# Optimization experiments

Hardware: AMD Instinct MI355X
Metric: run time of the kernel (lower is better)

The kernel has to match this reference:

```python
import jax, jax.numpy as jnp
import numpy as np

N_NODES = 100_000
N_EDGES = 1_000_000
LATENT = 64
HID_ATOM = 256
HID_BOND = 256
RBF_DIM = 32
RBF_DMAX = 10.0
N_ATOM_TYPES = 10
N_CHARGES = 6
N_BOND_ORDERS = 5


def setup_inputs() -> dict:
    key = jax.random.key(0)
    ks = jax.random.split(key, 12)
    positions = jax.random.normal(ks[0], (N_NODES, 3), dtype=jnp.float32) * 5.0
    quantized = jax.random.normal(ks[1], (N_NODES, LATENT), dtype=jnp.float32)
    pair_indices = jax.random.randint(ks[2], (N_EDGES, 2), 0, N_NODES, dtype=jnp.int64)
    s = 0.05
    return {
        "positions": positions,
        "quantized": quantized,
        "pair_indices": pair_indices,
        "aW1": jax.random.normal(ks[3], (LATENT, HID_ATOM), jnp.float32) * s,
        "ab1": jnp.zeros((HID_ATOM,), jnp.float32),
        "aW2": jax.random.normal(ks[4], (HID_ATOM, N_ATOM_TYPES + N_CHARGES), jnp.float32) * s,
        "ab2": jnp.zeros((N_ATOM_TYPES + N_CHARGES,), jnp.float32),
        "bW1": jax.random.normal(ks[5], (LATENT + RBF_DIM, HID_BOND), jnp.float32) * s,
        "bb1": jnp.zeros((HID_BOND,), jnp.float32),
        "bW2": jax.random.normal(ks[6], (HID_BOND, N_BOND_ORDERS), jnp.float32) * s,
        "bb2": jnp.zeros((N_BOND_ORDERS,), jnp.float32),
    }


def _norm_no_nan(x, eps=1e-8):
    # L2 norm over last axis, clamped to avoid NaN gradients at 0
    return jnp.sqrt(jnp.maximum(jnp.sum(x * x, axis=-1), eps))


def _rbf(D, D_min=0.0, D_max=RBF_DMAX, D_count=RBF_DIM):
    mu = jnp.linspace(D_min, D_max, D_count, dtype=D.dtype)  # [D_count]
    sigma = (D_max - D_min) / D_count
    z = (D[..., None] - mu) / sigma
    return jnp.exp(-z * z)  # [E, D_count]


def reference(positions, quantized, pair_indices, aW1, ab1, aW2, ab2, bW1, bb1, bW2, bb2):
    src = pair_indices[:, 0]
    dst = pair_indices[:, 1]
    # pairwise distances -> RBF expansion
    x_i = positions[src]            # [E, 3]
    x_j = positions[dst]
    dists = _rbf(_norm_no_nan(x_i - x_j))  # [E, rbf_dim]
    # atom decoder (per node)
    h = jax.nn.relu(quantized @ aW1 + ab1)
    scalar_logits = h @ aW2 + ab2
    atom_type_logits = scalar_logits[:, :N_ATOM_TYPES]
    atom_charge_logits = scalar_logits[:, N_ATOM_TYPES:]
    # bond decoder (per edge): gathered latent sum concat RBF
    pair_feats = quantized[src] + quantized[dst]           # [E, latent]
    combined = jnp.concatenate([pair_feats, dists], axis=1)  # [E, latent+rbf]
    hb = jax.nn.relu(combined @ bW1 + bb1)
    bond_order_logits = hb @ bW2 + bb2
    return (atom_type_logits, atom_charge_logits, bond_order_logits)
```

## Files before the change

### kernel.cpp

```cpp
#include <hip/hip_runtime.h>
#include <hip/hip_bf16.h>

typedef __bf16 bf16x8 __attribute__((ext_vector_type(8)));
typedef __bf16 bf16x4 __attribute__((ext_vector_type(4)));
typedef float  f32x4  __attribute__((ext_vector_type(4)));

#define N_NODES 100000
#define N_EDGES 1000000
#define LATENT  64
#define HID     256
#define RBF_DIM 32
#define NTYPES  10
#define NCHG    6
#define NBOND   5

#define ATOM_TILES (N_NODES / 32)
#define ANBLK 512

#define ETILE  64
#define ETILES (N_EDGES / ETILE)
#define ENBLK  512

__global__ __launch_bounds__(256) void prep_kernel(
    const float* __restrict__ q, __bf16* __restrict__ qb)
{
    const int i = blockIdx.x * 256 + threadIdx.x;
    const float4 a = *(const float4*)(q + (size_t)i * 8);
    const float4 b = *(const float4*)(q + (size_t)i * 8 + 4);
    bf16x8 v;
    v[0] = (__bf16)a.x; v[1] = (__bf16)a.y; v[2] = (__bf16)a.z; v[3] = (__bf16)a.w;
    v[4] = (__bf16)b.x; v[5] = (__bf16)b.y; v[6] = (__bf16)b.z; v[7] = (__bf16)b.w;
    *(bf16x8*)(qb + (size_t)i * 8) = v;
}

struct __align__(16) ASmem {
    __bf16 qs[32][72];
    __bf16 hsE[32][264];
    float  red[4][2][4][64];
};

__global__ __launch_bounds__(256, 2) void atom_kernel(
    const float* __restrict__ q,   const float* __restrict__ aW1,
    const float* __restrict__ ab1, const float* __restrict__ aW2,
    const float* __restrict__ ab2, float* __restrict__ outA,
    float* __restrict__ outB)
{
    __shared__ ASmem sm;
    const int t    = threadIdx.x;
    const int w    = t >> 6;
    const int lane = t & 63;
    const int l15  = lane & 15;
    const int hi   = lane >> 4;
    const int wcol = w * 64;

    bf16x8 aw1f[2][4];
    #pragma unroll
    for (int kb = 0; kb < 2; ++kb)
        #pragma unroll
        for (int nt = 0; nt < 4; ++nt) {
            const int nn = wcol + nt * 16 + l15;
            const int k0 = kb * 32 + hi * 8;
            bf16x8 v;
            #pragma unroll
            for (int j = 0; j < 8; ++j) v[j] = (__bf16)aW1[(k0 + j) * HID + nn];
            aw1f[kb][nt] = v;
        }
    bf16x8 aw2f[2];
    #pragma unroll
    for (int kk = 0; kk < 2; ++kk) {
        const int k0 = (w * 2 + kk) * 32 + hi * 8;
        bf16x8 v;
        #pragma unroll
        for (int j = 0; j < 8; ++j) v[j] = (__bf16)aW2[(k0 + j) * 16 + l15];
        aw2f[kk] = v;
    }
    float4 b1v[4];
    #pragma unroll
    for (int nt = 0; nt < 4; ++nt)
        b1v[nt] = *(const float4*)(&ab1[wcol + nt * 16 + hi * 4]);

    const int m_st = t >> 3;
    const int p_st = t & 7;

    for (int tile = blockIdx.x; tile < ATOM_TILES; tile += ANBLK) {
        const int node0 = tile * 32;
        {
            const float* qr = q + (size_t)(node0 + m_st) * 64 + p_st * 8;
            const float4 a0 = *(const float4*)(qr);
            const float4 a1 = *(const float4*)(qr + 4);
            bf16x8 v;
            v[0] = (__bf16)a0.x; v[1] = (__bf16)a0.y; v[2] = (__bf16)a0.z; v[3] = (__bf16)a0.w;
            v[4] = (__bf16)a1.x; v[5] = (__bf16)a1.y; v[6] = (__bf16)a1.z; v[7] = (__bf16)a1.w;
            *(bf16x8*)(&sm.qs[m_st][p_st * 8]) = v;
        }
        __syncthreads();

        f32x4 acc[2][4];
        #pragma unroll
        for (int mt = 0; mt < 2; ++mt)
            #pragma unroll
            for (int nt = 0; nt < 4; ++nt) {
                f32x4 z = {0.f, 0.f, 0.f, 0.f};
                acc[mt][nt] = z;
            }
        #pragma unroll
        for (int kb = 0; kb < 2; ++kb)
            #pragma unroll
            for (int mt = 0; mt < 2; ++mt) {
                const bf16x8 bq = *(const bf16x8*)((const char*)&sm.qs[0][0]
                                   + (mt * 16 + l15) * 144 + kb * 64 + hi * 16);
                #pragma unroll
                for (int nt = 0; nt < 4; ++nt)
                    acc[mt][nt] = __builtin_amdgcn_mfma_f32_16x16x32_bf16(
                        aw1f[kb][nt], bq, acc[mt][nt], 0, 0, 0);
            }
        #pragma unroll
        for (int mt = 0; mt < 2; ++mt)
            #pragma unroll
            for (int nt = 0; nt < 4; ++nt) {
                bf16x4 hv;
                #pragma unroll
                for (int r = 0; r < 4; ++r)
                    hv[r] = (__bf16)fmaxf(acc[mt][nt][r] + ((const float*)&b1v[nt])[r], 0.f);
                *(bf16x4*)(&sm.hsE[mt * 16 + l15][wcol + nt * 16 + hi * 4]) = hv;
            }
        __syncthreads();

        f32x4 acc2[2];
        {
            f32x4 z = {0.f, 0.f, 0.f, 0.f};
            acc2[0] = z; acc2[1] = z;
        }
        #pragma unroll
        for (int mt = 0; mt < 2; ++mt)
            #pragma unroll
            for (int kk = 0; kk < 2; ++kk) {
                const int kb = w * 2 + kk;
                const bf16x8 af = *(const bf16x8*)((const char*)&sm.hsE[0][0]
                                   + (mt * 16 + l15) * 528 + kb * 64 + hi * 16);
                acc2[mt] = __builtin_amdgcn_mfma_f32_16x16x32_bf16(
                    af, aw2f[kk], acc2[mt], 0, 0, 0);
            }
        #pragma unroll
        for (int mt = 0; mt < 2; ++mt)
            #pragma unroll
            for (int r = 0; r < 4; ++r)
                sm.red[w][mt][r][lane] = acc2[mt][r];
        __syncthreads();

        {
            const int o  = t & 15;
            const int m0 = t >> 4;
            #pragma unroll
            for (int half = 0; half < 2; ++half) {
                const int m  = m0 + half * 16;
                const int mt = m >> 4, rr = m & 15;
                const int hh = rr >> 2, r = rr & 3;
                float s = ab2[o];
                #pragma unroll
                for (int ww = 0; ww < 4; ++ww) s += sm.red[ww][mt][r][hh * 16 + o];
                const int node = node0 + m;
                if (o < NTYPES) outA[node * NTYPES + o] = s;
                else            outB[node * NCHG + (o - NTYPES)] = s;
            }
        }
        __syncthreads();
    }
}

struct __align__(16) ESmem {
    __bf16 comb[ETILE][104];
    __bf16 hsE[ETILE][264];
    __bf16 w2t[16][264];
};

template<bool USEBF>
__global__ __launch_bounds__(512, 4) void edge_kernel(
    const float* __restrict__ pos, const float* __restrict__ qf,
    const __bf16* __restrict__ qb, const int* __restrict__ pair,
    const float* __restrict__ bW1, const float* __restrict__ bb1,
    const float* __restrict__ bW2, const float* __restrict__ bb2,
    float* __restrict__ outC)
{
    __shared__ ESmem sm;
    const int t    = threadIdx.x;
    const int w    = t >> 6;
    const int lane = t & 63;
    const int l15  = lane & 15;
    const int hi   = lane >> 4;
    const int wcol = w * 32;

    {
        const int o  = t >> 5;
        const int k0 = (t & 31) * 8;
        bf16x8 v;
        #pragma unroll
        for (int j = 0; j < 8; ++j)
            v[j] = (o < NBOND) ? (__bf16)bW2[(k0 + j) * NBOND + o] : (__bf16)0.f;
        *(bf16x8*)(&sm.w2t[o][k0]) = v;
    }

    bf16x8 bw1f[3][2];
    #pragma unroll
    for (int kb = 0; kb < 3; ++kb)
        #pragma unroll
        for (int nt = 0; nt < 2; ++nt) {
            const int nn = wcol + nt * 16 + l15;
            const int k0 = kb * 32 + hi * 8;
            bf16x8 v;
            #pragma unroll
            for (int j = 0; j < 8; ++j) v[j] = (__bf16)bW1[(k0 + j) * HID + nn];
            bw1f[kb][nt] = v;
        }
    float4 b1v[2];
    b1v[0] = *(const float4*)(&bb1[wcol + hi * 4]);
    b1v[1] = *(const float4*)(&bb1[wcol + 16 + hi * 4]);
    const float bb2v = (l15 < NBOND) ? bb2[l15] : 0.f;

    const int e_loc = t >> 3;
    const int p     = t & 7;

    int tile = blockIdx.x;
    int2 pA = ((const int2*)pair)[(size_t)tile * ETILE + e_loc];
    bf16x8 gs, gd;
    float4 fs0, fs1, fd0, fd1;
    float  ps0, ps1, ps2, pd0, pd1, pd2;
    if constexpr (USEBF) {
        gs = *(const bf16x8*)(qb + (size_t)pA.x * 64 + p * 8);
        gd = *(const bf16x8*)(qb + (size_t)pA.y * 64 + p * 8);
    } else {
        fs0 = *(const float4*)(qf + (size_t)pA.x * 64 + p * 8);
        fs1 = *(const float4*)(qf + (size_t)pA.x * 64 + p * 8 + 4);
        fd0 = *(const float4*)(qf + (size_t)pA.y * 64 + p * 8);
        fd1 = *(const float4*)(qf + (size_t)pA.y * 64 + p * 8 + 4);
    }
    ps0 = pos[(size_t)pA.x * 3];  ps1 = pos[(size_t)pA.x * 3 + 1];  ps2 = pos[(size_t)pA.x * 3 + 2];
    pd0 = pos[(size_t)pA.y * 3];  pd1 = pos[(size_t)pA.y * 3 + 1];  pd2 = pos[(size_t)pA.y * 3 + 2];
    {
        const int tn = tile + ENBLK;
        pA = ((const int2*)pair)[(tn < ETILES ? (size_t)tn * ETILE : 0) + e_loc];
    }
    __syncthreads();

    for (; tile < ETILES; tile += ENBLK) {
        const int e0 = tile * ETILE;

        {
            bf16x8 cv;
            if constexpr (USEBF) {
                #pragma unroll
                for (int j = 0; j < 8; ++j)
                    cv[j] = (__bf16)((float)gs[j] + (float)gd[j]);
            } else {
                cv[0] = (__bf16)(fs0.x + fd0.x); cv[1] = (__bf16)(fs0.y + fd0.y);
                cv[2] = (__bf16)(fs0.z + fd0.z); cv[3] = (__bf16)(fs0.w + fd0.w);
                cv[4] = (__bf16)(fs1.x + fd1.x); cv[5] = (__bf16)(fs1.y + fd1.y);
                cv[6] = (__bf16)(fs1.z + fd1.z); cv[7] = (__bf16)(fs1.w + fd1.w);
            }
            *(bf16x8*)(&sm.comb[e_loc][p * 8]) = cv;

            const float dx = ps0 - pd0, dy = ps1 - pd1, dz = ps2 - pd2;
            const float D  = sqrtf(fmaxf(dx * dx + dy * dy + dz * dz, 1e-8f));
            bf16x4 rv;
            #pragma unroll
            for (int j = 0; j < 4; ++j) {
                const float mu = (float)(p * 4 + j) * (10.0f / 31.0f);
                const float z  = (D - mu) * 3.2f;
                rv[j] = (__bf16)__expf(-z * z);
            }
            *(bf16x4*)(&sm.comb[e_loc][64 + p * 4]) = rv;
        }
        __syncthreads();

        {
            const int2 pN = pA;
            if constexpr (USEBF) {
                gs = *(const bf16x8*)(qb + (size_t)pN.x * 64 + p * 8);
                gd = *(const bf16x8*)(qb + (size_t)pN.y * 64 + p * 8);
            } else {
                fs0 = *(const float4*)(qf + (size_t)pN.x * 64 + p * 8);
                fs1 = *(const float4*)(qf + (size_t)pN.x * 64 + p * 8 + 4);
                fd0 = *(const float4*)(qf + (size_t)pN.y * 64 + p * 8);
                fd1 = *(const float4*)(qf + (size_t)pN.y * 64 + p * 8 + 4);
            }
            ps0 = pos[(size_t)pN.x * 3];  ps1 = pos[(size_t)pN.x * 3 + 1];  ps2 = pos[(size_t)pN.x * 3 + 2];
            pd0 = pos[(size_t)pN.y * 3];  pd1 = pos[(size_t)pN.y * 3 + 1];  pd2 = pos[(size_t)pN.y * 3 + 2];
            const int tnn = tile + 2 * ENBLK;
            pA = ((const int2*)pair)[(tnn < ETILES ? (size_t)tnn * ETILE : 0) + e_loc];
        }

        f32x4 acc[4][2];
        #pragma unroll
        for (int mt = 0; mt < 4; ++mt)
            #pragma unroll
            for (int nt = 0; nt < 2; ++nt) {
                f32x4 z = {0.f, 0.f, 0.f, 0.f};
                acc[mt][nt] = z;
            }
        #pragma unroll
        for (int kb = 0; kb < 3; ++kb)
            #pragma unroll
            for (int mt = 0; mt < 4; ++mt) {
                const bf16x8 bf = *(const bf16x8*)((const char*)&sm.comb[0][0]
                                   + (mt * 16 + l15) * 208 + kb * 64 + hi * 16);
                acc[mt][0] = __builtin_amdgcn_mfma_f32_16x16x32_bf16(
                    bw1f[kb][0], bf, acc[mt][0], 0, 0, 0);
                acc[mt][1] = __builtin_amdgcn_mfma_f32_16x16x32_bf16(
                    bw1f[kb][1], bf, acc[mt][1], 0, 0, 0);
            }
        #pragma unroll
        for (int mt = 0; mt < 4; ++mt)
            #pragma unroll
            for (int nt = 0; nt < 2; ++nt) {
                bf16x4 hv;
                #pragma unroll
                for (int r = 0; r < 4; ++r)
                    hv[r] = (__bf16)fmaxf(acc[mt][nt][r] + ((const float*)&b1v[nt])[r], 0.f);
                *(bf16x4*)((char*)&sm.hsE[0][0]
                           + (mt * 16 + l15) * 528 + (wcol + nt * 16 + hi * 4) * 2) = hv;
            }
        __syncthreads();

        if (w < 4) {
            f32x4 a2a = {0.f, 0.f, 0.f, 0.f};
            f32x4 a2b = {0.f, 0.f, 0.f, 0.f};
            #pragma unroll
            for (int kk = 0; kk < 8; kk += 2) {
                const bf16x8 af0 = *(const bf16x8*)((const char*)&sm.hsE[0][0]
                                    + (w * 16 + l15) * 528 + kk * 64 + hi * 16);
                const bf16x8 bf0 = *(const bf16x8*)((const char*)&sm.w2t[0][0]
                                    + l15 * 528 + kk * 64 + hi * 16);
                a2a = __builtin_amdgcn_mfma_f32_16x16x32_bf16(af0, bf0, a2a, 0, 0, 0);
                const bf16x8 af1 = *(const bf16x8*)((const char*)&sm.hsE[0][0]
                                    + (w * 16 + l15) * 528 + (kk + 1) * 64 + hi * 16);
                const bf16x8 bf1 = *(const bf16x8*)((const char*)&sm.w2t[0][0]
                                    + l15 * 528 + (kk + 1) * 64 + hi * 16);
                a2b = __builtin_amdgcn_mfma_f32_16x16x32_bf16(af1, bf1, a2b, 0, 0, 0);
            }
            if (l15 < NBOND) {
                #pragma unroll
                for (int r = 0; r < 4; ++r)
                    outC[(size_t)(e0 + w * 16 + hi * 4 + r) * NBOND + l15]
                        = a2a[r] + a2b[r] + bb2v;
            }
        }
    }
}

extern "C" void kernel_launch(void* const* d_in, const int* in_sizes, int n_in,
                              void* d_out, int out_size, void* d_ws, size_t ws_size,
                              hipStream_t stream)
{
    const float* pos = (const float*)d_in[0];
    const float* q   = (const float*)d_in[1];
    const int*   pair= (const int*)  d_in[2];
    const float* aW1 = (const float*)d_in[3];
    const float* ab1 = (const float*)d_in[4];
    const float* aW2 = (const float*)d_in[5];
    const float* ab2 = (const float*)d_in[6];
    const float* bW1 = (const float*)d_in[7];
    const float* bb1 = (const float*)d_in[8];
    const float* bW2 = (const float*)d_in[9];
    const float* bb2 = (const float*)d_in[10];

    float* out  = (float*)d_out;
    float* outA = out;
    float* outB = out + (size_t)N_NODES * NTYPES;
    float* outC = out + (size_t)N_NODES * (NTYPES + NCHG);

    const size_t qb_bytes = (size_t)N_NODES * LATENT * sizeof(__bf16);
    const bool use_bf = (ws_size >= qb_bytes);
    __bf16* qb = (__bf16*)d_ws;

    if (use_bf)
        hipLaunchKernelGGL(prep_kernel, dim3(N_NODES * LATENT / (256 * 8)), dim3(256),
                           0, stream, q, qb);

    hipLaunchKernelGGL(atom_kernel, dim3(ANBLK), dim3(256), 0, stream,
                       q, aW1, ab1, aW2, ab2, outA, outB);

    if (use_bf)
        hipLaunchKernelGGL(edge_kernel<true>, dim3(ENBLK), dim3(512), 0, stream,
                           pos, q, qb, pair, bW1, bb1, bW2, bb2, outC);
    else
        hipLaunchKernelGGL(edge_kernel<false>, dim3(ENBLK), dim3(512), 0, stream,
                           pos, q, qb, pair, bW1, bb1, bW2, bb2, outC);
}
```

Baseline: 101.9 us.

## Swizzle edge-kernel LDS layouts, retile waves to 2x4, use lightweight barriers

Replaces the padded LDS rows in the edge kernel with unpadded power-of-two rows and XOR swizzling to avoid bank conflicts. It also changes the per-wave work split from 4 M-tiles by 2 N-tiles to 2 M-tiles by 4 N-tiles, so each comb fragment read from LDS feeds more MFMAs, at the cost of holding more weight fragments in registers. __syncthreads is replaced with an explicit lgkmcnt wait plus s_barrier, and the first barrier now sits after the next-tile gather loads are issued. The larger bw1f register array may pressure occupancy under the 512-thread, 4-block launch bounds.

```diff
diff --git a/kernel.cpp b/kernel.cpp
--- a/kernel.cpp
+++ b/kernel.cpp
@@ -169,10 +169,15 @@
 }
 
 struct __align__(16) ESmem {
-    __bf16 comb[ETILE][104];
-    __bf16 hsE[ETILE][264];
-    __bf16 w2t[16][264];
+    __bf16 comb[ETILE][128];
+    __bf16 hsE[ETILE][256];
+    __bf16 w2t[16][256];
 };
+
+__device__ __forceinline__ void bar_lgkm() {
+    asm volatile("s_waitcnt lgkmcnt(0)" ::: "memory");
+    __builtin_amdgcn_s_barrier();
+}
 
 template<bool USEBF>
 __global__ __launch_bounds__(512, 4) void edge_kernel(
@@ -188,37 +193,41 @@
     const int lane = t & 63;
     const int l15  = lane & 15;
     const int hi   = lane >> 4;
-    const int wcol = w * 32;
+    const int hid0 = (w & 3) * 64;
+    const int emg  = (w >> 2) * 32;
+    const int swz  = (l15 & 7) << 4;
 
     {
         const int o  = t >> 5;
-        const int k0 = (t & 31) * 8;
+        const int kq = t & 31;
         bf16x8 v;
         #pragma unroll
         for (int j = 0; j < 8; ++j)
-            v[j] = (o < NBOND) ? (__bf16)bW2[(k0 + j) * NBOND + o] : (__bf16)0.f;
-        *(bf16x8*)(&sm.w2t[o][k0]) = v;
-    }
-
-    bf16x8 bw1f[3][2];
+            v[j] = (o < NBOND) ? (__bf16)bW2[(kq * 8 + j) * NBOND + o] : (__bf16)0.f;
+        *(bf16x8*)((char*)&sm.w2t[0][0] + o * 512 + ((kq * 16) ^ ((o & 7) << 4))) = v;
+    }
+
+    bf16x8 bw1f[3][4];
     #pragma unroll
     for (int kb = 0; kb < 3; ++kb)
         #pragma unroll
-        for (int nt = 0; nt < 2; ++nt) {
-            const int nn = wcol + nt * 16 + l15;
+        for (int nt = 0; nt < 4; ++nt) {
+            const int nn = hid0 + nt * 16 + l15;
             const int k0 = kb * 32 + hi * 8;
             bf16x8 v;
             #pragma unroll
             for (int j = 0; j < 8; ++j) v[j] = (__bf16)bW1[(k0 + j) * HID + nn];
             bw1f[kb][nt] = v;
         }
-    float4 b1v[2];
-    b1v[0] = *(const float4*)(&bb1[wcol + hi * 4]);
-    b1v[1] = *(const float4*)(&bb1[wcol + 16 + hi * 4]);
+    float4 b1v[4];
+    #pragma unroll
+    for (int nt = 0; nt < 4; ++nt)
+        b1v[nt] = *(const float4*)(&bb1[hid0 + nt * 16 + hi * 4]);
     const float bb2v = (l15 < NBOND) ? bb2[l15] : 0.f;
 
     const int e_loc = t >> 3;
     const int p     = t & 7;
+    const int wswz  = (e_loc & 7) << 4;
 
     int tile = blockIdx.x;
     int2 pA = ((const int2*)pair)[(size_t)tile * ETILE + e_loc];
@@ -257,7 +266,7 @@
                 cv[4] = (__bf16)(fs1.x + fd1.x); cv[5] = (__bf16)(fs1.y + fd1.y);
                 cv[6] = (__bf16)(fs1.z + fd1.z); cv[7] = (__bf16)(fs1.w + fd1.w);
             }
-            *(bf16x8*)(&sm.comb[e_loc][p * 8]) = cv;
+            *(bf16x8*)((char*)&sm.comb[0][0] + e_loc * 256 + ((p * 16) ^ wswz)) = cv;
 
             const float dx = ps0 - pd0, dy = ps1 - pd1, dz = ps2 - pd2;
             const float D  = sqrtf(fmaxf(dx * dx + dy * dy + dz * dz, 1e-8f));
@@ -268,9 +277,8 @@
                 const float z  = (D - mu) * 3.2f;
                 rv[j] = (__bf16)__expf(-z * z);
             }
-            *(bf16x4*)(&sm.comb[e_loc][64 + p * 4]) = rv;
-        }
-        __syncthreads();
+            *(bf16x4*)((char*)&sm.comb[0][0] + e_loc * 256 + ((128 + p * 8) ^ wswz)) = rv;
+        }
 
         {
             const int2 pN = pA;
@@ -288,38 +296,41 @@
             const int tnn = tile + 2 * ENBLK;
             pA = ((const int2*)pair)[(tnn < ETILES ? (size_t)tnn * ETILE : 0) + e_loc];
         }
-
-        f32x4 acc[4][2];
-        #pragma unroll
-        for (int mt = 0; mt < 4; ++mt)
-            #pragma unroll
-            for (int nt = 0; nt < 2; ++nt) {
+        bar_lgkm();
+
+        f32x4 acc[2][4];
+        #pragma unroll
+        for (int mt = 0; mt < 2; ++mt)
+            #pragma unroll
+            for (int nt = 0; nt < 4; ++nt) {
                 f32x4 z = {0.f, 0.f, 0.f, 0.f};
                 acc[mt][nt] = z;
             }
         #pragma unroll
         for (int kb = 0; kb < 3; ++kb)
             #pragma unroll
-            for (int mt = 0; mt < 4; ++mt) {
+            for (int mt = 0; mt < 2; ++mt) {
                 const bf16x8 bf = *(const bf16x8*)((const char*)&sm.comb[0][0]
-                                   + (mt * 16 + l15) * 208 + kb * 64 + hi * 16);
-                acc[mt][0] = __builtin_amdgcn_mfma_f32_16x16x32_bf16(
-                    bw1f[kb][0], bf, acc[mt][0], 0, 0, 0);
-                acc[mt][1] = __builtin_amdgcn_mfma_f32_16x16x32_bf16(
-                    bw1f[kb][1], bf, acc[mt][1], 0, 0, 0);
-            }
-        #pragma unroll
-        for (int mt = 0; mt < 4; ++mt)
-            #pragma unroll
-            for (int nt = 0; nt < 2; ++nt) {
+                                   + (emg + mt * 16 + l15) * 256
+                                   + ((kb * 64 + hi * 16) ^ swz));
+                #pragma unroll
+                for (int nt = 0; nt < 4; ++nt)
+                    acc[mt][nt] = __builtin_amdgcn_mfma_f32_16x16x32_bf16(
+                        bw1f[kb][nt], bf, acc[mt][nt], 0, 0, 0);
+            }
+        #pragma unroll
+        for (int mt = 0; mt < 2; ++mt)
+            #pragma unroll
+            for (int nt = 0; nt < 4; ++nt) {
                 bf16x4 hv;
                 #pragma unroll
                 for (int r = 0; r < 4; ++r)
                     hv[r] = (__bf16)fmaxf(acc[mt][nt][r] + ((const float*)&b1v[nt])[r], 0.f);
                 *(bf16x4*)((char*)&sm.hsE[0][0]
-                           + (mt * 16 + l15) * 528 + (wcol + nt * 16 + hi * 4) * 2) = hv;
-            }
-        __syncthreads();
+                           + (emg + mt * 16 + l15) * 512
+                           + ((hid0 * 2 + nt * 32 + hi * 8) ^ swz)) = hv;
+            }
+        bar_lgkm();
 
         if (w < 4) {
             f32x4 a2a = {0.f, 0.f, 0.f, 0.f};
@@ -327,14 +338,14 @@
             #pragma unroll
             for (int kk = 0; kk < 8; kk += 2) {
                 const bf16x8 af0 = *(const bf16x8*)((const char*)&sm.hsE[0][0]
-                                    + (w * 16 + l15) * 528 + kk * 64 + hi * 16);
+                                    + (w * 16 + l15) * 512 + ((kk * 64 + hi * 16) ^ swz));
                 const bf16x8 bf0 = *(const bf16x8*)((const char*)&sm.w2t[0][0]
-                                    + l15 * 528 + kk * 64 + hi * 16);
+                                    + l15 * 512 + ((kk * 64 + hi * 16) ^ swz));
                 a2a = __builtin_amdgcn_mfma_f32_16x16x32_bf16(af0, bf0, a2a, 0, 0, 0);
                 const bf16x8 af1 = *(const bf16x8*)((const char*)&sm.hsE[0][0]
-                                    + (w * 16 + l15) * 528 + (kk + 1) * 64 + hi * 16);
+                                    + (w * 16 + l15) * 512 + (((kk + 1) * 64 + hi * 16) ^ swz));
                 const bf16x8 bf1 = *(const bf16x8*)((const char*)&sm.w2t[0][0]
-                                    + l15 * 528 + (kk + 1) * 64 + hi * 16);
+                                    + l15 * 512 + (((kk + 1) * 64 + hi * 16) ^ swz));
                 a2b = __builtin_amdgcn_mfma_f32_16x16x32_bf16(af1, bf1, a2b, 0, 0, 0);
             }
             if (l15 < NBOND) {
```

Result: slower. 232.5 us (+128.2%).
